# Performance work log

Hardware: AMD Instinct MI355X
Metric: run time of the kernel (lower is better)

## Reference

```python
import jax, jax.numpy as jnp
import numpy as np

HIDDEN = 2048
NUM_HEADS = 16
HEAD_DIM = HIDDEN // NUM_HEADS
SCALE = 1.0 / np.sqrt(HEAD_DIM).astype(np.float32)
BATCH, SEQ = 2, 2048


def setup_inputs() -> dict:
    key = jax.random.key(0)
    ks = jax.random.split(key, 9)
    std = 0.02
    inp = {
        'hidden_states': jax.random.normal(ks[0], (BATCH, SEQ, HIDDEN), jnp.float32),
        'attention_mask': jnp.zeros((BATCH, 1, 1, SEQ), jnp.float32),
        'Wq': jax.random.normal(ks[1], (HIDDEN, HIDDEN), jnp.float32) * std,
        'bq': jnp.zeros((HIDDEN,), jnp.float32),
        'Wk': jax.random.normal(ks[2], (HIDDEN, HIDDEN), jnp.float32) * std,
        'bk': jnp.zeros((HIDDEN,), jnp.float32),
        'Wv': jax.random.normal(ks[3], (HIDDEN, HIDDEN), jnp.float32) * std,
        'bv': jnp.zeros((HIDDEN,), jnp.float32),
        'Wo': jax.random.normal(ks[4], (HIDDEN, HIDDEN), jnp.float32) * std,
        'bo': jnp.zeros((HIDDEN,), jnp.float32),
    }
    return inp


def _split_heads(x):
    b, s, _ = x.shape
    return x.reshape(b, s, NUM_HEADS, HEAD_DIM).transpose(0, 2, 1, 3)  # [b,h,s,d]


def reference(hidden_states, attention_mask, Wq, bq, Wk, bk, Wv, bv, Wo, bo):
    # Linear layers (torch convention: y = x @ W.T + b)
    q = _split_heads(hidden_states @ Wq.T + bq)
    k = _split_heads(hidden_states @ Wk.T + bk)
    v = _split_heads(hidden_states @ Wv.T + bv)
    scores = jnp.einsum('bhqd,bhkd->bhqk', q, k) * SCALE
    scores = scores + attention_mask
    weights = jax.nn.softmax(scores, axis=-1)  # dropout is identity in eval
    ctx = jnp.einsum('bhqk,bhkd->bhqd', weights, v)
    b, h, s, d = ctx.shape
    ctx = ctx.transpose(0, 2, 1, 3).reshape(b, s, HIDDEN)
    return ctx @ Wo.T + bo
```

## Files before the change

### kernel.cpp

```cpp
#include <hip/hip_runtime.h>

typedef __bf16 bf16_t;
typedef bf16_t bf16x8 __attribute__((ext_vector_type(8)));
typedef float f32x4 __attribute__((ext_vector_type(4)));

#define HIDDEN 2048
#define SEQ 2048
#define BATCH 2
#define NHEADS 16
#define HDIM 128
#define MTOT (BATCH*SEQ)
#define SCALE 0.088388347648318447f
#define C1EXP2 0.12753102158508967f
#define LOG2E  1.4426950408889634f

__device__ __forceinline__ float dev_exp2(float x) { return __builtin_amdgcn_exp2f(x); }

typedef __attribute__((address_space(1))) const void gvoid_t;
typedef __attribute__((address_space(3))) void svoid_t;
__device__ __forceinline__ void async_copy16(const bf16_t* g, bf16_t* l) {
  __builtin_amdgcn_global_load_lds((gvoid_t*)g, (svoid_t*)l, 16, 0, 0);
}

__global__ void cvt_all(const float* __restrict__ x,  const float* __restrict__ wq,
                        const float* __restrict__ wk, const float* __restrict__ wv,
                        const float* __restrict__ wo,
                        bf16_t* __restrict__ xb, bf16_t* __restrict__ wqkb,
                        bf16_t* __restrict__ wvb, bf16_t* __restrict__ wob) {
  const size_t HH = (size_t)HIDDEN * HIDDEN;
  const float* src; bf16_t* dst;
  switch (blockIdx.y) {
    case 0:  src = x;        dst = xb;        break;
    case 1:  src = x + HH;   dst = xb + HH;   break;
    case 2:  src = wq;       dst = wqkb;      break;
    case 3:  src = wk;       dst = wqkb + HH; break;
    case 4:  src = wv;       dst = wvb;       break;
    default: src = wo;       dst = wob;       break;
  }
  int i = blockIdx.x * 256 + threadIdx.x;
  float4 v = reinterpret_cast<const float4*>(src)[i];
  union { bf16_t h[4]; uint2 u; } t;
  t.h[0] = (bf16_t)v.x; t.h[1] = (bf16_t)v.y; t.h[2] = (bf16_t)v.z; t.h[3] = (bf16_t)v.w;
  reinterpret_cast<uint2*>(dst)[i] = t.u;
}

__global__ void pack_bias2(const float* __restrict__ a, const float* __restrict__ b2,
                           float* __restrict__ out) {
  int i = blockIdx.x * 256 + threadIdx.x;
  out[i] = (i < HIDDEN) ? a[i] : b2[i - HIDDEN];
}

#define QKK 2048
#define RD_A(dst, buf, mh) do {                                                \
  _Pragma("unroll") for (int mi_ = 0; mi_ < 4; ++mi_)                          \
    _Pragma("unroll") for (int kk_ = 0; kk_ < 2; ++kk_)                        \
      dst[mi_][kk_] = *(const bf16x8*)&As[buf][mh][(wr * 64 + mi_ * 16 + lr) * 64 \
                         + (((kk_ * 4 + quad) ^ (lr & 7)) * 8)];               \
} while (0)
#define RD_B(dst, buf, nh) do {                                                \
  _Pragma("unroll") for (int ni_ = 0; ni_ < 2; ++ni_)                          \
    _Pragma("unroll") for (int kk_ = 0; kk_ < 2; ++kk_)                        \
      dst[ni_][kk_] = *(const bf16x8*)&Bs[buf][nh][(wc * 32 + ni_ * 16 + lr) * 64 \
                         + (((kk_ * 4 + quad) ^ (lr & 7)) * 8)];               \
} while (0)
#define MMQ(mh, nh, afr, bfr) do {                                             \
  __builtin_amdgcn_s_setprio(1);                                               \
  _Pragma("unroll") for (int mi_ = 0; mi_ < 4; ++mi_)                          \
    _Pragma("unroll") for (int ni_ = 0; ni_ < 2; ++ni_) {                      \
      acc[(mh)*4 + mi_][(nh)*2 + ni_] = __builtin_amdgcn_mfma_f32_16x16x32_bf16( \
          afr[mi_][0], bfr[ni_][0], acc[(mh)*4 + mi_][(nh)*2 + ni_], 0, 0, 0); \
      acc[(mh)*4 + mi_][(nh)*2 + ni_] = __builtin_amdgcn_mfma_f32_16x16x32_bf16( \
          afr[mi_][1], bfr[ni_][1], acc[(mh)*4 + mi_][(nh)*2 + ni_], 0, 0, 0); \
    }                                                                          \
  __builtin_amdgcn_s_setprio(0);                                               \
} while (0)
#define STG(ptr, t64, ldsbase) do {                                            \
  async_copy16((ptr) + (t64), (ldsbase));                                      \
  async_copy16((ptr) + (size_t)8 * QKK + (t64), (ldsbase) + 8 * 64);           \
} while (0)
#define PHASE_SYNC do { __builtin_amdgcn_s_barrier();                          \
  asm volatile("s_waitcnt lgkmcnt(0)" ::: "memory");                           \
  __builtin_amdgcn_sched_barrier(0); } while (0)

__global__ __launch_bounds__(512)
void gemm8p(const bf16_t* __restrict__ A, const bf16_t* __restrict__ Bt,
            const float* __restrict__ bias, bf16_t* __restrict__ Y) {
  __shared__ __align__(16) bf16_t As[2][2][128 * 64];
  __shared__ __align__(16) bf16_t Bs[2][2][128 * 64];
  const int tid  = threadIdx.x;
  const int lane = tid & 63;
  const int wv   = tid >> 6;
  const int wr   = wv >> 2, wc = wv & 3;
  const int lr   = lane & 15, quad = lane >> 4;

  const int wg  = blockIdx.x;
  const int swz = (wg & 7) * 32 + (wg >> 3);
  const int m0  = (swz >> 4) * 256;
  const int n0  = (swz & 15) * 256;

  f32x4 acc[8][4] = {};

  const int sub = lane >> 3, chv = (lane & 7) ^ sub;
  const int rih = wv * 16 + sub;
  const bf16_t* pA0 = A  + (size_t)(m0 +       rih) * QKK + chv * 8;
  const bf16_t* pA1 = A  + (size_t)(m0 + 128 + rih) * QKK + chv * 8;
  const bf16_t* pB0 = Bt + (size_t)(n0 +       rih) * QKK + chv * 8;
  const bf16_t* pB1 = Bt + (size_t)(n0 + 128 + rih) * QKK + chv * 8;
  const int lwo = wv * 16 * 64;
  const int nt  = QKK >> 6;

  STG(pB0, (size_t)0,  &Bs[0][0][lwo]);
  STG(pA0, (size_t)0,  &As[0][0][lwo]);
  STG(pA1, (size_t)0,  &As[0][1][lwo]);
  STG(pB1, (size_t)0,  &Bs[0][1][lwo]);
  STG(pB0, (size_t)64, &Bs[1][0][lwo]);
  STG(pA0, (size_t)64, &As[1][0][lwo]);
  asm volatile("s_waitcnt vmcnt(2)" ::: "memory");
  __builtin_amdgcn_s_barrier();

  bf16x8 afr[4][2], bf0[2][2], bf1[2][2];

  for (int t = 0; t < nt; ++t) {
    const int p = t & 1;
    const size_t tk = (size_t)t * 64;

    RD_A(afr, p, 0); RD_B(bf0, p, 0);
    if (t + 1 < nt) STG(pA1, tk + 64, &As[p ^ 1][1][lwo]);
    PHASE_SYNC; MMQ(0, 0, afr, bf0); __builtin_amdgcn_s_barrier();

    RD_B(bf1, p, 1);
    if (t + 1 < nt) STG(pB1, tk + 64, &Bs[p ^ 1][1][lwo]);
    PHASE_SYNC; MMQ(0, 1, afr, bf1); __builtin_amdgcn_s_barrier();

    RD_A(afr, p, 1);
    if (t + 2 < nt) STG(pB0, tk + 128, &Bs[p][0][lwo]);
    PHASE_SYNC; MMQ(1, 1, afr, bf1); __builtin_amdgcn_s_barrier();

    if (t + 2 < nt) {
      STG(pA0, tk + 128, &As[p][0][lwo]);
      asm volatile("s_waitcnt vmcnt(4)" ::: "memory");
    } else {
      asm volatile("s_waitcnt vmcnt(0)" ::: "memory");
    }
    PHASE_SYNC; MMQ(1, 0, afr, bf0); __builtin_amdgcn_s_barrier();
  }

  float bc[4];
#pragma unroll
  for (int fn = 0; fn < 4; ++fn)
    bc[fn] = bias[n0 + (fn >> 1) * 128 + wc * 32 + (fn & 1) * 16 + lr];
#pragma unroll
  for (int fm = 0; fm < 8; ++fm) {
    const int rowb = m0 + (fm >> 2) * 128 + wr * 64 + (fm & 3) * 16 + quad * 4;
#pragma unroll
    for (int r = 0; r < 4; ++r) {
      const size_t base = (size_t)(rowb + r) * 4096;
#pragma unroll
      for (int fn = 0; fn < 4; ++fn) {
        const int col = n0 + (fn >> 1) * 128 + wc * 32 + (fn & 1) * 16 + lr;
        Y[base + col] = (bf16_t)(acc[fm][fn][r] + bc[fn]);
      }
    }
  }
}

#define TSTG(ptr, t64, ldsbase) do {                                           \
  async_copy16((ptr) + (t64), (ldsbase));                                      \
  async_copy16((ptr) + (size_t)8 * K + (t64), (ldsbase) + 8 * 64);             \
} while (0)
#define TRD(kk) do {                                                           \
  _Pragma("unroll") for (int fi_ = 0; fi_ < 4; ++fi_)                          \
    af[fi_] = *(const bf16x8*)&As[buf][(wr * 64 + fi_ * 16 + lr) * 64          \
                  + ((((kk) * 4 + quad) ^ (lr & 7)) * 8)];                     \
  _Pragma("unroll") for (int fi_ = 0; fi_ < 4; ++fi_)                          \
    bf[fi_] = *(const bf16x8*)&Bs[buf][(wc * 64 + fi_ * 16 + lr) * 64          \
                  + ((((kk) * 4 + quad) ^ (lr & 7)) * 8)];                     \
} while (0)
#define TMM() do {                                                             \
  __builtin_amdgcn_s_setprio(1);                                               \
  _Pragma("unroll") for (int fm_ = 0; fm_ < 4; ++fm_)                          \
    _Pragma("unroll") for (int fn_ = 0; fn_ < 4; ++fn_)                        \
      acc[fm_][fn_] = __builtin_amdgcn_mfma_f32_16x16x32_bf16(                 \
          af[fm_], bf[fn_], acc[fm_][fn_], 0, 0, 0);                           \
  __builtin_amdgcn_s_setprio(0);                                               \
} while (0)

template<bool OUT_BF16, bool ROW_BIAS>
__global__ __launch_bounds__(512)
void gemm_tall(const bf16_t* __restrict__ A, const bf16_t* __restrict__ Bt,
               const float* __restrict__ bias, void* __restrict__ Yv,
               int K, int ldY, int nbt) {
  __shared__ __align__(16) bf16_t As[3][256 * 64];
  __shared__ __align__(16) bf16_t Bs[3][128 * 64];
  const int tid  = threadIdx.x;
  const int lane = tid & 63;
  const int wv   = tid >> 6;
  const int wr   = wv >> 1, wc = wv & 1;
  const int lr   = lane & 15, quad = lane >> 4;

  const int wg  = blockIdx.x;
  const int swz = (wg & 7) * 32 + (wg >> 3);
  const int m0  = (swz / nbt) * 256;
  const int n0  = (swz % nbt) * 128;

  f32x4 acc[4][4] = {};

  const int sub = lane >> 3, chv = (lane & 7) ^ sub;
  const int rih = wv * 16 + sub;
  const bf16_t* pA = A  + (size_t)(m0 + rih) * K + chv * 8;
  const bf16_t* pB = Bt + (size_t)(n0 + rih) * K + chv * 8;
  const size_t a1off = (size_t)128 * K;
  const int lwo = wv * 16 * 64;
  const int nt  = K >> 6;

  TSTG(pA,         (size_t)0,  &As[0][lwo]);
  TSTG(pA + a1off, (size_t)0,  &As[0][128 * 64 + lwo]);
  TSTG(pB,         (size_t)0,  &Bs[0][lwo]);
  TSTG(pA,         (size_t)64, &As[1][lwo]);
  TSTG(pA + a1off, (size_t)64, &As[1][128 * 64 + lwo]);
  TSTG(pB,         (size_t)64, &Bs[1][lwo]);
  asm volatile("s_waitcnt vmcnt(6)" ::: "memory");
  __builtin_amdgcn_s_barrier();

  bf16x8 af[4], bf[4];
  for (int t = 0; t < nt; ++t) {
    const int buf = t % 3;

    TRD(0);
    if (t + 2 < nt) {
      const int b2 = (buf < 1) ? buf + 2 : buf - 1;
      const size_t tk2 = (size_t)(t + 2) * 64;
      TSTG(pA,         tk2, &As[b2][lwo]);
      TSTG(pA + a1off, tk2, &As[b2][128 * 64 + lwo]);
      TSTG(pB,         tk2, &Bs[b2][lwo]);
    }
    PHASE_SYNC; TMM(); __builtin_amdgcn_s_barrier();

    TRD(1);
    if (t + 2 < nt) { asm volatile("s_waitcnt vmcnt(6)" ::: "memory"); }
    else            { asm volatile("s_waitcnt vmcnt(0)" ::: "memory"); }
    PHASE_SYNC; TMM(); __builtin_amdgcn_s_barrier();
  }

  float bc[4];
  if (!ROW_BIAS) {
#pragma unroll
    for (int fn = 0; fn < 4; ++fn) bc[fn] = bias[n0 + wc * 64 + fn * 16 + lr];
  }
#pragma unroll
  for (int fm = 0; fm < 4; ++fm) {
    const int rowb = m0 + wr * 64 + fm * 16 + quad * 4;
#pragma unroll
    for (int r = 0; r < 4; ++r) {
      const int row = rowb + r;
      const float brow = ROW_BIAS ? bias[row] : 0.0f;
      const size_t base = (size_t)row * ldY;
#pragma unroll
      for (int fn = 0; fn < 4; ++fn) {
        const int col = n0 + wc * 64 + fn * 16 + lr;
        float y = acc[fm][fn][r] + (ROW_BIAS ? brow : bc[fn]);
        if (OUT_BF16) ((bf16_t*)Yv)[base + col] = (bf16_t)y;
        else          ((float*)Yv)[base + col]  = y;
      }
    }
  }
}

#define BQ 256
#define BKV 64
#define LDQK 4096

__global__ __launch_bounds__(512)
void attn_kernel(const bf16_t* __restrict__ QK, const bf16_t* __restrict__ Vt,
                 const float* __restrict__ mask, bf16_t* __restrict__ O) {
  __shared__ __align__(16) bf16_t Ks[2][BKV * 128];
  __shared__ __align__(16) bf16_t Vs[2][HDIM * BKV];
  __shared__ __align__(16) bf16_t Ps[BQ * BKV];
  __shared__ __align__(16) float  Msk[SEQ];

  const int tid  = threadIdx.x;
  const int lane = tid & 63;
  const int wv   = tid >> 6;
  const int lr   = lane & 15, quad = lane >> 4;
  const int q0   = blockIdx.x * BQ;
  const int bh   = blockIdx.y;
  const int b    = bh >> 4, h = bh & 15;

  const bf16_t* Qg = QK + (size_t)(b * SEQ + q0) * LDQK + h * HDIM;
  const bf16_t* Kg = QK + (size_t)(b * SEQ) * LDQK + HIDDEN + h * HDIM;
  const bf16_t* Vg = Vt + (size_t)(h * HDIM) * MTOT + b * SEQ;
  const float*  mb = mask + b * SEQ;

  bf16x8 qf[2][4];
#pragma unroll
  for (int mi = 0; mi < 2; ++mi)
#pragma unroll
    for (int dk = 0; dk < 4; ++dk)
      qf[mi][dk] = *(const bf16x8*)(Qg + (size_t)(wv * 32 + mi * 16 + lr) * LDQK + dk * 32 + quad * 8);

  for (int i = tid; i < SEQ / 4; i += 512) {
    float4 mv = reinterpret_cast<const float4*>(mb)[i];
    Msk[i * 4 + 0] = mv.x * LOG2E;
    Msk[i * 4 + 1] = mv.y * LOG2E;
    Msk[i * 4 + 2] = mv.z * LOG2E;
    Msk[i * 4 + 3] = mv.w * LOG2E;
  }

  const int kcs = lane & 15;
  const int vcs = lane & 7;
  const bf16_t* kgp[2]; const bf16_t* vgp[2];
  int lKo[2], lVo[2];
#pragma unroll
  for (int i = 0; i < 2; ++i) {
    int kr = wv * 8 + i * 4 + (lane >> 4);
    kgp[i] = Kg + (size_t)kr * LDQK + ((kcs ^ (kr & 15)) * 8);
    lKo[i] = (wv * 8 + i * 4) * 128;
    int vr = wv * 16 + i * 8 + (lane >> 3);
    vgp[i] = Vg + (size_t)vr * MTOT + ((vcs ^ (vr & 7)) * 8);
    lVo[i] = (wv * 16 + i * 8) * 64;
  }

  asm volatile("s_waitcnt vmcnt(0)" ::: "memory");
#pragma unroll
  for (int i = 0; i < 2; ++i) async_copy16(kgp[i], &Ks[0][lKo[i]]);
#pragma unroll
  for (int i = 0; i < 2; ++i) async_copy16(vgp[i], &Vs[0][lVo[i]]);
  asm volatile("s_waitcnt lgkmcnt(0)" ::: "memory");
  __builtin_amdgcn_s_barrier();

  float l_st[2][4] = {};
  f32x4 oacc[2][8] = {};

  for (int kt = 0; kt < SEQ; kt += BKV) {
    const int cur = (kt >> 6) & 1;
    const bf16_t* Kc = &Ks[cur][0];
    const bf16_t* Vc = &Vs[cur][0];

    asm volatile("s_waitcnt lgkmcnt(0)" ::: "memory");
    __builtin_amdgcn_s_barrier();
    if (kt + BKV < SEQ) {
#pragma unroll
      for (int i = 0; i < 2; ++i)
        async_copy16(kgp[i] + (size_t)(kt + BKV) * LDQK, &Ks[cur ^ 1][lKo[i]]);
#pragma unroll
      for (int i = 0; i < 2; ++i)
        async_copy16(vgp[i] + (kt + BKV), &Vs[cur ^ 1][lVo[i]]);
      asm volatile("s_waitcnt vmcnt(4)" ::: "memory");
    } else {
      asm volatile("s_waitcnt vmcnt(0)" ::: "memory");
    }
    __builtin_amdgcn_s_barrier();
    __builtin_amdgcn_sched_barrier(0);

    float mk[4];
#pragma unroll
    for (int ni = 0; ni < 4; ++ni) mk[ni] = Msk[kt + ni * 16 + lr];

    f32x4 sacc[2][4] = {};
#pragma unroll
    for (int dk = 0; dk < 4; ++dk) {
      bf16x8 kf[4];
#pragma unroll
      for (int ni = 0; ni < 4; ++ni)
        kf[ni] = *(const bf16x8*)&Kc[(ni * 16 + lr) * 128 + (((dk * 4 + quad) ^ lr) * 8)];
#pragma unroll
      for (int mi = 0; mi < 2; ++mi)
#pragma unroll
        for (int ni = 0; ni < 4; ++ni)
          sacc[mi][ni] = __builtin_amdgcn_mfma_f32_16x16x32_bf16(qf[mi][dk], kf[ni], sacc[mi][ni], 0, 0, 0);
    }

#pragma unroll
    for (int mi = 0; mi < 2; ++mi) {
#pragma unroll
      for (int r = 0; r < 4; ++r) {
        float p0 = dev_exp2(fmaf(sacc[mi][0][r], C1EXP2, mk[0]));
        float p1 = dev_exp2(fmaf(sacc[mi][1][r], C1EXP2, mk[1]));
        float p2 = dev_exp2(fmaf(sacc[mi][2][r], C1EXP2, mk[2]));
        float p3 = dev_exp2(fmaf(sacc[mi][3][r], C1EXP2, mk[3]));
        int pr = wv * 32 + mi * 16 + quad * 4 + r;
        int key = pr & 7;
        Ps[pr * BKV + (((0 + (lr >> 3)) ^ key) * 8) + (lr & 7)] = (bf16_t)p0;
        Ps[pr * BKV + (((2 + (lr >> 3)) ^ key) * 8) + (lr & 7)] = (bf16_t)p1;
        Ps[pr * BKV + (((4 + (lr >> 3)) ^ key) * 8) + (lr & 7)] = (bf16_t)p2;
        Ps[pr * BKV + (((6 + (lr >> 3)) ^ key) * 8) + (lr & 7)] = (bf16_t)p3;
        l_st[mi][r] += (p0 + p1) + (p2 + p3);
      }
    }

#pragma unroll
    for (int ki = 0; ki < 2; ++ki) {
      bf16x8 pf[2];
#pragma unroll
      for (int mi = 0; mi < 2; ++mi)
        pf[mi] = *(const bf16x8*)&Ps[(wv * 32 + mi * 16 + lr) * BKV + (((ki * 4 + quad) ^ (lr & 7)) * 8)];
#pragma unroll
      for (int di = 0; di < 8; ++di) {
        bf16x8 vf = *(const bf16x8*)&Vc[(di * 16 + lr) * BKV + (((ki * 4 + quad) ^ (lr & 7)) * 8)];
#pragma unroll
        for (int mi = 0; mi < 2; ++mi)
          oacc[mi][di] = __builtin_amdgcn_mfma_f32_16x16x32_bf16(pf[mi], vf, oacc[mi][di], 0, 0, 0);
      }
    }
  }

  bf16_t* Ob = O + (size_t)(b * SEQ + q0) * HIDDEN + h * HDIM;
#pragma unroll
  for (int mi = 0; mi < 2; ++mi) {
#pragma unroll
    for (int r = 0; r < 4; ++r) {
      float s = l_st[mi][r];
      s += __shfl_xor(s, 1);
      s += __shfl_xor(s, 2);
      s += __shfl_xor(s, 4);
      s += __shfl_xor(s, 8);
      float inv = 1.0f / s;
      size_t rowoff = (size_t)(wv * 32 + mi * 16 + quad * 4 + r) * HIDDEN;
#pragma unroll
      for (int di = 0; di < 8; ++di)
        Ob[rowoff + di * 16 + lr] = (bf16_t)(oacc[mi][di][r] * inv);
    }
  }
}

extern "C" void kernel_launch(void* const* d_in, const int* in_sizes, int n_in,
                              void* d_out, int out_size, void* d_ws, size_t ws_size,
                              hipStream_t stream) {
  const float* x   = (const float*)d_in[0];
  const float* msk = (const float*)d_in[1];
  const float* Wq  = (const float*)d_in[2];
  const float* bq  = (const float*)d_in[3];
  const float* Wk  = (const float*)d_in[4];
  const float* bk  = (const float*)d_in[5];
  const float* Wv  = (const float*)d_in[6];
  const float* bv  = (const float*)d_in[7];
  const float* Wo  = (const float*)d_in[8];
  const float* bo  = (const float*)d_in[9];
  float* out = (float*)d_out;

  bf16_t* Xb   = (bf16_t*)d_ws;
  bf16_t* Wqkb = Xb   + (size_t)MTOT * HIDDEN;
  bf16_t* Wvb  = Wqkb + (size_t)2 * HIDDEN * HIDDEN;
  bf16_t* Wob  = Wvb  + (size_t)HIDDEN * HIDDEN;
  bf16_t* QKo  = Wob  + (size_t)HIDDEN * HIDDEN;
  bf16_t* Vto  = QKo  + (size_t)MTOT * 2 * HIDDEN;
  float*  bqk  = (float*)(Vto + (size_t)HIDDEN * MTOT);
  bf16_t* Cb   = Xb;

  cvt_all<<<dim3(HIDDEN * HIDDEN / 4 / 256, 6), 256, 0, stream>>>(
      x, Wq, Wk, Wv, Wo, Xb, Wqkb, Wvb, Wob);
  pack_bias2<<<2 * HIDDEN / 256, 256, 0, stream>>>(bq, bk, bqk);

  gemm8p<<<256, 512, 0, stream>>>(Xb, Wqkb, bqk, QKo);
  gemm_tall<true, true><<<256, 512, 0, stream>>>(Wvb, Xb, bv, Vto, HIDDEN, 4096, 32);
  attn_kernel<<<dim3(SEQ / BQ, BATCH * NHEADS), 512, 0, stream>>>(QKo, Vto, msk, Cb);
  gemm_tall<false, false><<<256, 512, 0, stream>>>(Cb, Wob, bo, out, HIDDEN, 2048, 16);
}
```

Measured before the change: 404.7 us.

## Replace QK projection GEMM with 256x128 triple-buffered BK=32 kernel; raise MFMA priority in attention

Replaces the 256x256 tile, BK=64 double-buffered QK projection GEMM with a templated 256x128 tile, BK=32 kernel using a three-stage LDS ring. The grid grows to 512 blocks and occupancy is hinted at 4 blocks per CU. The goal is to fill the CUs better and keep more loads in flight. Separately, the attention kernel wraps its MFMA blocks in s_setprio to favour matrix issue over the other waves. The trade-offs are less data reuse per tile and more barriers per K step.

```diff
diff --git a/kernel.cpp b/kernel.cpp
--- a/kernel.cpp
+++ b/kernel.cpp
@@ -50,115 +50,111 @@
   out[i] = (i < HIDDEN) ? a[i] : b2[i - HIDDEN];
 }
 
-#define QKK 2048
-#define RD_A(dst, buf, mh) do {                                                \
-  _Pragma("unroll") for (int mi_ = 0; mi_ < 4; ++mi_)                          \
-    _Pragma("unroll") for (int kk_ = 0; kk_ < 2; ++kk_)                        \
-      dst[mi_][kk_] = *(const bf16x8*)&As[buf][mh][(wr * 64 + mi_ * 16 + lr) * 64 \
-                         + (((kk_ * 4 + quad) ^ (lr & 7)) * 8)];               \
-} while (0)
-#define RD_B(dst, buf, nh) do {                                                \
-  _Pragma("unroll") for (int ni_ = 0; ni_ < 2; ++ni_)                          \
-    _Pragma("unroll") for (int kk_ = 0; kk_ < 2; ++kk_)                        \
-      dst[ni_][kk_] = *(const bf16x8*)&Bs[buf][nh][(wc * 32 + ni_ * 16 + lr) * 64 \
-                         + (((kk_ * 4 + quad) ^ (lr & 7)) * 8)];               \
-} while (0)
-#define MMQ(mh, nh, afr, bfr) do {                                             \
-  __builtin_amdgcn_s_setprio(1);                                               \
-  _Pragma("unroll") for (int mi_ = 0; mi_ < 4; ++mi_)                          \
-    _Pragma("unroll") for (int ni_ = 0; ni_ < 2; ++ni_) {                      \
-      acc[(mh)*4 + mi_][(nh)*2 + ni_] = __builtin_amdgcn_mfma_f32_16x16x32_bf16( \
-          afr[mi_][0], bfr[ni_][0], acc[(mh)*4 + mi_][(nh)*2 + ni_], 0, 0, 0); \
-      acc[(mh)*4 + mi_][(nh)*2 + ni_] = __builtin_amdgcn_mfma_f32_16x16x32_bf16( \
-          afr[mi_][1], bfr[ni_][1], acc[(mh)*4 + mi_][(nh)*2 + ni_], 0, 0, 0); \
-    }                                                                          \
-  __builtin_amdgcn_s_setprio(0);                                               \
-} while (0)
-#define STG(ptr, t64, ldsbase) do {                                            \
-  async_copy16((ptr) + (t64), (ldsbase));                                      \
-  async_copy16((ptr) + (size_t)8 * QKK + (t64), (ldsbase) + 8 * 64);           \
-} while (0)
 #define PHASE_SYNC do { __builtin_amdgcn_s_barrier();                          \
   asm volatile("s_waitcnt lgkmcnt(0)" ::: "memory");                           \
   __builtin_amdgcn_sched_barrier(0); } while (0)
 
-__global__ __launch_bounds__(512)
-void gemm8p(const bf16_t* __restrict__ A, const bf16_t* __restrict__ Bt,
-            const float* __restrict__ bias, bf16_t* __restrict__ Y) {
-  __shared__ __align__(16) bf16_t As[2][2][128 * 64];
-  __shared__ __align__(16) bf16_t Bs[2][2][128 * 64];
+template<bool OUT_BF16, bool ROW_BIAS>
+__global__ __launch_bounds__(512, 4)
+void gemm32(const bf16_t* __restrict__ A, const bf16_t* __restrict__ Bt,
+            const float* __restrict__ bias, void* __restrict__ Yv,
+            int K, int ldY, int nbt) {
+  __shared__ __align__(16) bf16_t As[3][256 * 32];
+  __shared__ __align__(16) bf16_t Bs[3][128 * 32];
   const int tid  = threadIdx.x;
   const int lane = tid & 63;
   const int wv   = tid >> 6;
-  const int wr   = wv >> 2, wc = wv & 3;
+  const int wr   = wv >> 1, wc = wv & 1;
   const int lr   = lane & 15, quad = lane >> 4;
+  const int kx   = (lr >> 1) & 3;
 
   const int wg  = blockIdx.x;
-  const int swz = (wg & 7) * 32 + (wg >> 3);
-  const int m0  = (swz >> 4) * 256;
-  const int n0  = (swz & 15) * 256;
-
-  f32x4 acc[8][4] = {};
-
-  const int sub = lane >> 3, chv = (lane & 7) ^ sub;
-  const int rih = wv * 16 + sub;
-  const bf16_t* pA0 = A  + (size_t)(m0 +       rih) * QKK + chv * 8;
-  const bf16_t* pA1 = A  + (size_t)(m0 + 128 + rih) * QKK + chv * 8;
-  const bf16_t* pB0 = Bt + (size_t)(n0 +       rih) * QKK + chv * 8;
-  const bf16_t* pB1 = Bt + (size_t)(n0 + 128 + rih) * QKK + chv * 8;
-  const int lwo = wv * 16 * 64;
-  const int nt  = QKK >> 6;
-
-  STG(pB0, (size_t)0,  &Bs[0][0][lwo]);
-  STG(pA0, (size_t)0,  &As[0][0][lwo]);
-  STG(pA1, (size_t)0,  &As[0][1][lwo]);
-  STG(pB1, (size_t)0,  &Bs[0][1][lwo]);
-  STG(pB0, (size_t)64, &Bs[1][0][lwo]);
-  STG(pA0, (size_t)64, &As[1][0][lwo]);
-  asm volatile("s_waitcnt vmcnt(2)" ::: "memory");
+  const int cpx = gridDim.x >> 3;
+  const int swz = (wg & 7) * cpx + (wg >> 3);
+  const int m0  = (swz / nbt) * 256;
+  const int n0  = (swz % nbt) * 128;
+
+  f32x4 acc[4][4] = {};
+
+  const int srow = lane >> 2;
+  const int sch  = (lane & 3) ^ ((lane >> 3) & 3);
+  const bf16_t* pA0 = A  + (size_t)(m0 +       wv * 16 + srow) * K + sch * 8;
+  const bf16_t* pA1 = A  + (size_t)(m0 + 128 + wv * 16 + srow) * K + sch * 8;
+  const bf16_t* pB  = Bt + (size_t)(n0 +       wv * 16 + srow) * K + sch * 8;
+  const int lA0 = (wv * 16) * 32, lA1 = (128 + wv * 16) * 32, lB = (wv * 16) * 32;
+  const int nt = K >> 5;
+
+  async_copy16(pA0,      &As[0][lA0]);
+  async_copy16(pA1,      &As[0][lA1]);
+  async_copy16(pB,       &Bs[0][lB]);
+  async_copy16(pA0 + 32, &As[1][lA0]);
+  async_copy16(pA1 + 32, &As[1][lA1]);
+  async_copy16(pB  + 32, &Bs[1][lB]);
+  asm volatile("s_waitcnt vmcnt(3)" ::: "memory");
   __builtin_amdgcn_s_barrier();
 
-  bf16x8 afr[4][2], bf0[2][2], bf1[2][2];
-
+  bf16x8 af[4], bfr[2];
   for (int t = 0; t < nt; ++t) {
-    const int p = t & 1;
-    const size_t tk = (size_t)t * 64;
-
-    RD_A(afr, p, 0); RD_B(bf0, p, 0);
-    if (t + 1 < nt) STG(pA1, tk + 64, &As[p ^ 1][1][lwo]);
-    PHASE_SYNC; MMQ(0, 0, afr, bf0); __builtin_amdgcn_s_barrier();
-
-    RD_B(bf1, p, 1);
-    if (t + 1 < nt) STG(pB1, tk + 64, &Bs[p ^ 1][1][lwo]);
-    PHASE_SYNC; MMQ(0, 1, afr, bf1); __builtin_amdgcn_s_barrier();
-
-    RD_A(afr, p, 1);
-    if (t + 2 < nt) STG(pB0, tk + 128, &Bs[p][0][lwo]);
-    PHASE_SYNC; MMQ(1, 1, afr, bf1); __builtin_amdgcn_s_barrier();
-
+    const int buf = t % 3;
+
+#pragma unroll
+    for (int mi = 0; mi < 4; ++mi)
+      af[mi] = *(const bf16x8*)&As[buf][(wr * 64 + mi * 16 + lr) * 32 + ((quad ^ kx) * 8)];
+#pragma unroll
+    for (int ni = 0; ni < 2; ++ni)
+      bfr[ni] = *(const bf16x8*)&Bs[buf][(wc * 64 + ni * 16 + lr) * 32 + ((quad ^ kx) * 8)];
     if (t + 2 < nt) {
-      STG(pA0, tk + 128, &As[p][0][lwo]);
-      asm volatile("s_waitcnt vmcnt(4)" ::: "memory");
-    } else {
-      asm volatile("s_waitcnt vmcnt(0)" ::: "memory");
-    }
-    PHASE_SYNC; MMQ(1, 0, afr, bf0); __builtin_amdgcn_s_barrier();
+      const int b2 = (buf < 1) ? buf + 2 : buf - 1;
+      const int ko = (t + 2) * 32;
+      async_copy16(pA0 + ko, &As[b2][lA0]);
+      async_copy16(pA1 + ko, &As[b2][lA1]);
+      async_copy16(pB  + ko, &Bs[b2][lB]);
+    }
+    PHASE_SYNC;
+    __builtin_amdgcn_s_setprio(1);
+#pragma unroll
+    for (int mi = 0; mi < 4; ++mi)
+#pragma unroll
+      for (int ni = 0; ni < 2; ++ni)
+        acc[mi][ni] = __builtin_amdgcn_mfma_f32_16x16x32_bf16(af[mi], bfr[ni], acc[mi][ni], 0, 0, 0);
+    __builtin_amdgcn_s_setprio(0);
+    __builtin_amdgcn_s_barrier();
+
+#pragma unroll
+    for (int ni = 0; ni < 2; ++ni)
+      bfr[ni] = *(const bf16x8*)&Bs[buf][(wc * 64 + (2 + ni) * 16 + lr) * 32 + ((quad ^ kx) * 8)];
+    if (t + 2 < nt) { asm volatile("s_waitcnt vmcnt(3)" ::: "memory"); }
+    else            { asm volatile("s_waitcnt vmcnt(0)" ::: "memory"); }
+    PHASE_SYNC;
+    __builtin_amdgcn_s_setprio(1);
+#pragma unroll
+    for (int mi = 0; mi < 4; ++mi)
+#pragma unroll
+      for (int ni = 0; ni < 2; ++ni)
+        acc[mi][2 + ni] = __builtin_amdgcn_mfma_f32_16x16x32_bf16(af[mi], bfr[ni], acc[mi][2 + ni], 0, 0, 0);
+    __builtin_amdgcn_s_setprio(0);
+    __builtin_amdgcn_s_barrier();
   }
 
   float bc[4];
-#pragma unroll
-  for (int fn = 0; fn < 4; ++fn)
-    bc[fn] = bias[n0 + (fn >> 1) * 128 + wc * 32 + (fn & 1) * 16 + lr];
-#pragma unroll
-  for (int fm = 0; fm < 8; ++fm) {
-    const int rowb = m0 + (fm >> 2) * 128 + wr * 64 + (fm & 3) * 16 + quad * 4;
+  if (!ROW_BIAS) {
+#pragma unroll
+    for (int fn = 0; fn < 4; ++fn) bc[fn] = bias[n0 + wc * 64 + fn * 16 + lr];
+  }
+#pragma unroll
+  for (int fm = 0; fm < 4; ++fm) {
+    const int rowb = m0 + wr * 64 + fm * 16 + quad * 4;
 #pragma unroll
     for (int r = 0; r < 4; ++r) {
-      const size_t base = (size_t)(rowb + r) * 4096;
+      const int row = rowb + r;
+      const float brow = ROW_BIAS ? bias[row] : 0.0f;
+      const size_t base = (size_t)row * ldY;
 #pragma unroll
       for (int fn = 0; fn < 4; ++fn) {
-        const int col = n0 + (fn >> 1) * 128 + wc * 32 + (fn & 1) * 16 + lr;
-        Y[base + col] = (bf16_t)(acc[fm][fn][r] + bc[fn]);
+        const int col = n0 + wc * 64 + fn * 16 + lr;
+        float y = acc[fm][fn][r] + (ROW_BIAS ? brow : bc[fn]);
+        if (OUT_BF16) ((bf16_t*)Yv)[base + col] = (bf16_t)y;
+        else          ((float*)Yv)[base + col]  = y;
       }
     }
   }
@@ -363,11 +359,13 @@
 #pragma unroll
       for (int ni = 0; ni < 4; ++ni)
         kf[ni] = *(const bf16x8*)&Kc[(ni * 16 + lr) * 128 + (((dk * 4 + quad) ^ lr) * 8)];
+      __builtin_amdgcn_s_setprio(1);
 #pragma unroll
       for (int mi = 0; mi < 2; ++mi)
 #pragma unroll
         for (int ni = 0; ni < 4; ++ni)
           sacc[mi][ni] = __builtin_amdgcn_mfma_f32_16x16x32_bf16(qf[mi][dk], kf[ni], sacc[mi][ni], 0, 0, 0);
+      __builtin_amdgcn_s_setprio(0);
     }
 
 #pragma unroll
@@ -397,9 +395,11 @@
 #pragma unroll
       for (int di = 0; di < 8; ++di) {
         bf16x8 vf = *(const bf16x8*)&Vc[(di * 16 + lr) * BKV + (((ki * 4 + quad) ^ (lr & 7)) * 8)];
+        __builtin_amdgcn_s_setprio(1);
 #pragma unroll
         for (int mi = 0; mi < 2; ++mi)
           oacc[mi][di] = __builtin_amdgcn_mfma_f32_16x16x32_bf16(pf[mi], vf, oacc[mi][di], 0, 0, 0);
+        __builtin_amdgcn_s_setprio(0);
       }
     }
   }
@@ -451,7 +451,7 @@
       x, Wq, Wk, Wv, Wo, Xb, Wqkb, Wvb, Wob);
   pack_bias2<<<2 * HIDDEN / 256, 256, 0, stream>>>(bq, bk, bqk);
 
-  gemm8p<<<256, 512, 0, stream>>>(Xb, Wqkb, bqk, QKo);
+  gemm32<true, false><<<512, 512, 0, stream>>>(Xb, Wqkb, bqk, QKo, HIDDEN, 4096, 32);
   gemm_tall<true, true><<<256, 512, 0, stream>>>(Wvb, Xb, bv, Vto, HIDDEN, 4096, 32);
   attn_kernel<<<dim3(SEQ / BQ, BATCH * NHEADS), 512, 0, stream>>>(QKo, Vto, msk, Cb);
   gemm_tall<false, false><<<256, 512, 0, stream>>>(Cb, Wob, bo, out, HIDDEN, 2048, 16);
```

New measurement: 410.5 us. No clear change (+1.4%).
